# Optimization experiments

Measured on AMD Instinct MI355X. Metric: run time of the kernel, lower is better.

## Reference

```python
import jax, jax.numpy as jnp
import numpy as np

NPOINT, RADIUS, NSAMPLE = 1024, 0.4, 32
BN_EPS = 1e-5


def fps(xyz, npoint):
    # xyz: [B, N, 3]. Deterministic start at index 0 (torch uses randint).
    B, N, _ = xyz.shape

    def step(carry, _):
        distance, farthest = carry  # [B,N], [B]
        centroid = jnp.take_along_axis(xyz, farthest[:, None, None], axis=1)  # [B,1,3]
        dist = jnp.sum((xyz - centroid) ** 2, -1)  # [B,N]
        distance = jnp.minimum(distance, dist)
        new_far = jnp.argmax(distance, axis=-1).astype(jnp.int32)
        return (distance, new_far), farthest

    init = (jnp.full((B, N), 1e10, xyz.dtype), jnp.zeros((B,), jnp.int32))
    _, cents = jax.lax.scan(step, init, None, length=npoint)  # [npoint, B]
    return cents.T  # [B, npoint]


def square_distance(src, dst):
    # src [B,S,3], dst [B,N,3] -> [B,S,N]
    d = -2.0 * jnp.einsum('bsc,bnc->bsn', src, dst)
    d = d + jnp.sum(src ** 2, -1)[:, :, None] + jnp.sum(dst ** 2, -1)[:, None, :]
    return jnp.clip(d, 1e-12, None)


def query_ball_point(radius, nsample, xyz, new_xyz):
    B, N, _ = xyz.shape
    S = new_xyz.shape[1]
    sqr = square_distance(new_xyz, xyz)  # [B,S,N]
    gi = jnp.where(sqr > radius ** 2, N, jnp.arange(N, dtype=jnp.int32)[None, None, :])
    gi = jnp.sort(gi, axis=-1)[:, :, :nsample]  # [B,S,K]
    first = gi[:, :, :1]
    return jnp.where(gi == N, first, gi)


def gather_points(points, idx):
    # points [B,N,C], idx [B,S,K] -> [B,S,K,C]
    B, S, K = idx.shape
    C = points.shape[-1]
    flat = jnp.take_along_axis(points, idx.reshape(B, S * K)[:, :, None], axis=1)
    return flat.reshape(B, S, K, C)


def setup_inputs() -> dict:
    key = jax.random.key(0)
    ks = jax.random.split(key, 10)
    B, N, D = 8, 4096, 64
    inp = {
        'xyz': jax.random.normal(ks[0], (B, 3, N), jnp.float32),
        'points': jax.random.normal(ks[1], (B, D, N), jnp.float32),
    }
    chans = [67, 64, 64, 128]
    for i in range(3):
        cin, cout = chans[i], chans[i + 1]
        inp[f'W{i}'] = jax.random.normal(ks[2 + i], (cout, cin), jnp.float32) * (1.0 / np.sqrt(cin))
        inp[f'b{i}'] = jnp.zeros((cout,), jnp.float32)
        inp[f'g{i}'] = jnp.ones((cout,), jnp.float32)
        inp[f'bt{i}'] = jnp.zeros((cout,), jnp.float32)
    return inp


def _forward(xyz, points, Ws, bs, gs, bts):
    xyz_t = jnp.transpose(xyz, (0, 2, 1))      # [B,N,3]
    pts_t = jnp.transpose(points, (0, 2, 1))   # [B,N,D]
    B, N, _ = xyz_t.shape

    fps_idx = fps(xyz_t, NPOINT)                              # [B,S]
    new_xyz = jnp.take_along_axis(xyz_t, fps_idx[:, :, None], axis=1)  # [B,S,3]
    idx = query_ball_point(RADIUS, NSAMPLE, xyz_t, new_xyz)   # [B,S,K]

    grouped_xyz = gather_points(xyz_t, idx)                   # [B,S,K,3]
    grouped_xyz_norm = grouped_xyz - new_xyz[:, :, None, :]
    grouped_pts = gather_points(pts_t, idx)                   # [B,S,K,D]
    new_points = jnp.concatenate([grouped_xyz_norm, grouped_pts], -1)  # [B,S,K,3+D]

    x = jnp.transpose(new_points, (0, 3, 2, 1))  # [B,C,K,S]
    for W, b, g, bt in zip(Ws, bs, gs, bts):
        x = jnp.einsum('oc,bcks->boks', W, x) + b[None, :, None, None]
        mean = jnp.mean(x, axis=(0, 2, 3), keepdims=True)
        var = jnp.var(x, axis=(0, 2, 3), keepdims=True)
        x = (x - mean) * jax.lax.rsqrt(var + BN_EPS)
        x = x * g[None, :, None, None] + bt[None, :, None, None]
        x = jax.nn.relu(x)
    out = jnp.max(x, axis=2)                      # [B,C_out,S]
    return jnp.transpose(new_xyz, (0, 2, 1)), out


def reference(xyz, points, W0, b0, g0, bt0, W1, b1, g1, bt1, W2, b2, g2, bt2):
    return _forward(xyz, points, (W0, W1, W2), (b0, b1, b2), (g0, g1, g2), (bt0, bt1, bt2))
```

## Files before the change

kernel.cpp:

```cpp
#include <hip/hip_runtime.h>
#include <cstddef>
#include <cstdint>

#define NB 8
#define NPTS 4096
#define NS 1024
#define NK 32
#define ND 64

typedef __attribute__((ext_vector_type(8))) short bf16x8;
typedef __attribute__((ext_vector_type(4))) float f32x4;

__device__ __forceinline__ short f2bf(float f) {
  unsigned u = __float_as_uint(f);
  u += 0x7FFF + ((u >> 16) & 1);
  return (short)(u >> 16);
}

__device__ __forceinline__ float bf2f(unsigned short u) {
  return __uint_as_float((unsigned)u << 16);
}

#define DPP_IMAX(v, ctrl)                                                     \
  {                                                                           \
    int _o = __builtin_amdgcn_update_dpp(v, v, ctrl, 0xf, 0xf, false);        \
    v = (_o > v) ? _o : v;                                                    \
  }

#define DPP_U64MAX(hi, lo, ctrl)                                              \
  {                                                                           \
    unsigned _nh = (unsigned)__builtin_amdgcn_update_dpp((int)(hi), (int)(hi),\
                                                         ctrl, 0xf, 0xf, false);\
    unsigned _nl = (unsigned)__builtin_amdgcn_update_dpp((int)(lo), (int)(lo),\
                                                         ctrl, 0xf, 0xf, false);\
    bool _gt = (_nh > (hi)) || (_nh == (hi) && _nl > (lo));                   \
    hi = _gt ? _nh : (hi);                                                    \
    lo = _gt ? _nl : (lo);                                                    \
  }

#define DPP_RED16(v, OP)                                                      \
  {                                                                           \
    int _i;                                                                   \
    _i = __builtin_amdgcn_update_dpp(__float_as_int(v), __float_as_int(v), 0x111, 0xf, 0xf, false); \
    v = OP(v, __int_as_float(_i));                                            \
    _i = __builtin_amdgcn_update_dpp(__float_as_int(v), __float_as_int(v), 0x112, 0xf, 0xf, false); \
    v = OP(v, __int_as_float(_i));                                            \
    _i = __builtin_amdgcn_update_dpp(__float_as_int(v), __float_as_int(v), 0x114, 0xf, 0xf, false); \
    v = OP(v, __int_as_float(_i));                                            \
    _i = __builtin_amdgcn_update_dpp(__float_as_int(v), __float_as_int(v), 0x118, 0xf, 0xf, false); \
    v = OP(v, __int_as_float(_i));                                            \
  }

__device__ __forceinline__ float fadd_op(float a, float b) { return a + b; }

__global__ __launch_bounds__(512) void fps_pgemm_kernel(
    const float* __restrict__ xyz, float* __restrict__ out_newxyz,
    float* __restrict__ ws_newxyz, const float* __restrict__ points,
    const float* __restrict__ W0, const float* __restrict__ b0g,
    unsigned short* __restrict__ P1) {
  __shared__ __align__(16) char smem[69760];
  const int t = threadIdx.x;

  if (blockIdx.x < 8) {
    float4* sXYZ4 = (float4*)smem;
    volatile unsigned long long* vRed =
        (volatile unsigned long long*)(smem + 65536);
    int* sWidx = (int*)(smem + 65664);
    const int b = blockIdx.x;
    const int wave = t >> 6;
    const int lane = t & 63;
    const float* xb = xyz + (size_t)b * 3 * NPTS;

    for (int i = t; i < NPTS; i += 512) {
      sXYZ4[i] = make_float4(xb[i], xb[NPTS + i], xb[2 * NPTS + i], 0.f);
    }
    if (t == 0) sWidx[0] = 0;
    if (t < 16) vRed[t] = 0xFFFFFFFFFFFFFFFFull;

    float px[8], py[8], pz[8], dist[8];
    {
      float4 a0 = ((const float4*)xb)[2 * t];
      float4 a1 = ((const float4*)xb)[2 * t + 1];
      float4 b0v = ((const float4*)(xb + NPTS))[2 * t];
      float4 b1v = ((const float4*)(xb + NPTS))[2 * t + 1];
      float4 c0 = ((const float4*)(xb + 2 * NPTS))[2 * t];
      float4 c1 = ((const float4*)(xb + 2 * NPTS))[2 * t + 1];
      px[0] = a0.x; px[1] = a0.y; px[2] = a0.z; px[3] = a0.w;
      px[4] = a1.x; px[5] = a1.y; px[6] = a1.z; px[7] = a1.w;
      py[0] = b0v.x; py[1] = b0v.y; py[2] = b0v.z; py[3] = b0v.w;
      py[4] = b1v.x; py[5] = b1v.y; py[6] = b1v.z; py[7] = b1v.w;
      pz[0] = c0.x; pz[1] = c0.y; pz[2] = c0.z; pz[3] = c0.w;
      pz[4] = c1.x; pz[5] = c1.y; pz[6] = c1.z; pz[7] = c1.w;
    }
#pragma unroll
    for (int j = 0; j < 8; ++j) dist[j] = 1e10f;

    float cx = xb[0], cy = xb[NPTS], cz = xb[2 * NPTS];

    __syncthreads();

    for (int s = 0; s < NS - 1; ++s) {
#pragma unroll
      for (int j = 0; j < 8; ++j) {
        float dx = __fadd_rn(px[j], -cx);
        float dy = __fadd_rn(py[j], -cy);
        float dz = __fadd_rn(pz[j], -cz);
        float d = __fadd_rn(__fadd_rn(__fmul_rn(dx, dx), __fmul_rn(dy, dy)),
                            __fmul_rn(dz, dz));
        dist[j] = fminf(dist[j], d);
      }
      float m = fmaxf(fmaxf(fmaxf(dist[0], dist[1]), fmaxf(dist[2], dist[3])),
                      fmaxf(fmaxf(dist[4], dist[5]), fmaxf(dist[6], dist[7])));
      int v = __float_as_int(m);
      DPP_IMAX(v, 0x111)
      DPP_IMAX(v, 0x112)
      DPP_IMAX(v, 0x114)
      DPP_IMAX(v, 0x118)
      DPP_IMAX(v, 0x142)
      DPP_IMAX(v, 0x143)
      const int wm_i = __builtin_amdgcn_readlane(v, 63);
      const float wm = __int_as_float(wm_i);
      unsigned long long claim = __ballot(m == wm);
      int firstlane = __ffsll(claim) - 1;
      const int par = s & 1;
      if (lane == firstlane) {
        int j = 7;
#pragma unroll
        for (int jj = 6; jj >= 0; --jj)
          if (dist[jj] == wm) j = jj;
        unsigned widx = (unsigned)(t * 8 + j);
        unsigned lo = ((unsigned)s << 12) | (4095u - widx);
        vRed[par * 8 + wave] =
            ((unsigned long long)(unsigned)wm_i << 32) | (unsigned long long)lo;
      }
      unsigned long long k;
      for (;;) {
        k = vRed[par * 8 + (lane & 7)];
        bool ok = (((unsigned)k) >> 12) == (unsigned)s;
        if (__ballot(ok) == ~0ull) break;
      }
      unsigned h2 = (unsigned)(k >> 32), l2 = (unsigned)k;
      float4 scoord;
      if (lane < 8) scoord = sXYZ4[4095 - (int)(l2 & 0xFFFu)];
      DPP_U64MAX(h2, l2, 0x111)
      DPP_U64MAX(h2, l2, 0x112)
      DPP_U64MAX(h2, l2, 0x114)
      const unsigned gl = (unsigned)__builtin_amdgcn_readlane((int)l2, 7);
      const int widx = 4095 - (int)(gl & 0xFFFu);
      const int wslot = widx >> 9;
      cx = __int_as_float(__builtin_amdgcn_readlane(__float_as_int(scoord.x), wslot));
      cy = __int_as_float(__builtin_amdgcn_readlane(__float_as_int(scoord.y), wslot));
      cz = __int_as_float(__builtin_amdgcn_readlane(__float_as_int(scoord.z), wslot));
      if (t == 0) sWidx[s + 1] = widx;
    }
    __syncthreads();
    for (int s2 = t; s2 < NS; s2 += 512) {
      int w = sWidx[s2];
      float4 c = sXYZ4[w];
      out_newxyz[b * 3 * NS + s2] = c.x;
      out_newxyz[b * 3 * NS + NS + s2] = c.y;
      out_newxyz[b * 3 * NS + 2 * NS + s2] = c.z;
      ws_newxyz[((b << 10) + s2) * 3 + 0] = c.x;
      ws_newxyz[((b << 10) + s2) * 3 + 1] = c.y;
      ws_newxyz[((b << 10) + s2) * 3 + 2] = c.z;
    }
  } else {
    float* sP = (float*)smem;
    float* sW = (float*)(smem + 16384);
    float* sB = (float*)(smem + 33792);
    const int blk = blockIdx.x - 8;
    const int bb = blk >> 6;
    const int n0 = (blk & 63) * 64;
    const float* pb = points + (size_t)bb * ND * NPTS;
    for (int f = t; f < 4096; f += 512) {
      int c = f >> 6, n = f & 63;
      sP[f] = pb[c * NPTS + n0 + n];
    }
    for (int f = t; f < 4096; f += 512) {
      int c = f >> 6, o = f & 63;
      sW[c * 68 + o] = W0[o * 67 + 3 + c];
    }
    if (t < 64) sB[t] = b0g[t];
    __syncthreads();
    if (t < 256) {
      const int nl = (t & 15) * 4;
      const int ol = (t >> 4) * 4;
      float acc[4][4];
#pragma unroll
      for (int i = 0; i < 4; ++i)
#pragma unroll
        for (int j = 0; j < 4; ++j) acc[i][j] = 0.f;
#pragma unroll 4
      for (int c = 0; c < 64; ++c) {
        float4 xv = *(const float4*)(sP + c * 64 + nl);
        float4 wv = *(const float4*)(sW + c * 68 + ol);
        float xa[4] = {xv.x, xv.y, xv.z, xv.w};
        float wa[4] = {wv.x, wv.y, wv.z, wv.w};
#pragma unroll
        for (int i = 0; i < 4; ++i)
#pragma unroll
          for (int j = 0; j < 4; ++j) acc[i][j] += xa[i] * wa[j];
      }
#pragma unroll
      for (int i = 0; i < 4; ++i) {
        ushort4 v;
        v.x = (unsigned short)f2bf(acc[i][0] + sB[ol + 0]);
        v.y = (unsigned short)f2bf(acc[i][1] + sB[ol + 1]);
        v.z = (unsigned short)f2bf(acc[i][2] + sB[ol + 2]);
        v.w = (unsigned short)f2bf(acc[i][3] + sB[ol + 3]);
        *(ushort4*)(P1 + ((size_t)(bb << 12) + n0 + nl + i) * 64 + ol) = v;
      }
    }
  }
}

__global__ __launch_bounds__(256) void query_gstats_kernel(
    const float* __restrict__ xyz, const float* __restrict__ ws_newxyz,
    const unsigned short* __restrict__ P1, const float* __restrict__ W0,
    unsigned short* __restrict__ y0g, float* __restrict__ partials) {
  const int w = threadIdx.x >> 6;
  const int lane = threadIdx.x & 63;
  const int p = blockIdx.x * 4 + w;
  const int b = p >> 10;
  __shared__ int sIdx[4][32];
  __shared__ float sWS[4][64];
  __shared__ float sWQ[4][64];
  const float* xb = xyz + (size_t)b * 3 * NPTS;
  const float cx = ws_newxyz[p * 3 + 0];
  const float cy = ws_newxyz[p * 3 + 1];
  const float cz = ws_newxyz[p * 3 + 2];
  const float ss = __fadd_rn(__fadd_rn(__fmul_rn(cx, cx), __fmul_rn(cy, cy)), __fmul_rn(cz, cz));
  const float r2 = (float)(0.4 * 0.4);
  int cnt = 0;
  for (int ci = 0; ci < 64 && cnt < 32; ++ci) {
    int n = ci * 64 + lane;
    float x = xb[n], y = xb[NPTS + n], z = xb[2 * NPTS + n];
    float dot = __fadd_rn(__fadd_rn(__fmul_rn(cx, x), __fmul_rn(cy, y)), __fmul_rn(cz, z));
    float dd = __fadd_rn(__fadd_rn(__fmul_rn(x, x), __fmul_rn(y, y)), __fmul_rn(z, z));
    float d = __fmul_rn(-2.0f, dot);
    d = __fadd_rn(d, ss);
    d = __fadd_rn(d, dd);
    d = fmaxf(d, 1e-12f);
    bool inc = (d <= r2);
    unsigned long long m = __ballot(inc);
    int slot = cnt + (int)__popcll(m & ((1ull << lane) - 1ull));
    if (inc && slot < 32) sIdx[w][slot] = n;
    cnt += (int)__popcll(m);
  }
  if (lane < 32) {
    int v;
    if (lane < cnt) v = sIdx[w][lane];
    else v = (cnt > 0) ? sIdx[w][0] : 0;
    sIdx[w][lane] = v;
  }
  const float wx = W0[lane * 67 + 0];
  const float wy = W0[lane * 67 + 1];
  const float wz = W0[lane * 67 + 2];
  float ssum = 0.f, ssq = 0.f;
  unsigned short* y0p = y0g + (size_t)p * 2048;
  for (int r = 0; r < 32; ++r) {
    const int n = sIdx[w][r];
    float P1v = bf2f(P1[((size_t)(b << 12) + n) * 64 + lane]);
    float dx = __fadd_rn(xb[n], -cx);
    float dy = __fadd_rn(xb[NPTS + n], -cy);
    float dz = __fadd_rn(xb[2 * NPTS + n], -cz);
    float y = P1v + (dx * wx + dy * wy + dz * wz);
    y0p[r * 64 + lane] = (unsigned short)f2bf(y);
    ssum += y;
    ssq += y * y;
  }
  sWS[w][lane] = ssum;
  sWQ[w][lane] = ssq;
  __syncthreads();
  const int t = threadIdx.x;
  if (t < 64) {
    float s1 = sWS[0][t] + sWS[1][t] + sWS[2][t] + sWS[3][t];
    float s2 = sWQ[0][t] + sWQ[1][t] + sWQ[2][t] + sWQ[3][t];
    partials[(size_t)blockIdx.x * 128 + t] = s1;
    partials[(size_t)blockIdx.x * 128 + 64 + t] = s2;
  }
}

__global__ __launch_bounds__(256) void conv1_mfma_kernel(
    const unsigned short* __restrict__ y0, const float* __restrict__ W1,
    const float* __restrict__ b1, const float* __restrict__ scaleA,
    const float* __restrict__ shiftA, unsigned short* __restrict__ y1,
    float* __restrict__ partials) {
  __shared__ __align__(16) short sW1b[64 * 72];
  __shared__ __align__(16) short sXb[128 * 72];
  __shared__ float sScale[64], sShift[64], sBias[64];

  const int t = threadIdx.x;
  const int wv = t >> 6, lane = t & 63;
  const int quad = lane >> 4, l15 = lane & 15;
  const int pair0 = blockIdx.x * 4;

  if (t < 64) { sScale[t] = scaleA[t]; sShift[t] = shiftA[t]; sBias[t] = b1[t]; }
  for (int f = t; f < 4096; f += 256) sW1b[(f >> 6) * 72 + (f & 63)] = f2bf(W1[f]);
  __syncthreads();

  const unsigned short* y0b = y0 + (size_t)pair0 * 2048;
  for (int f = t; f < 2048; f += 256) {
    ushort4 v4 = ((const ushort4*)y0b)[f];
    const int row = f >> 4, c4 = (f & 15) * 4;
    short4 o4;
    o4.x = f2bf(fmaxf(bf2f(v4.x) * sScale[c4 + 0] + sShift[c4 + 0], 0.f));
    o4.y = f2bf(fmaxf(bf2f(v4.y) * sScale[c4 + 1] + sShift[c4 + 1], 0.f));
    o4.z = f2bf(fmaxf(bf2f(v4.z) * sScale[c4 + 2] + sShift[c4 + 2], 0.f));
    o4.w = f2bf(fmaxf(bf2f(v4.w) * sScale[c4 + 3] + sShift[c4 + 3], 0.f));
    *(short4*)(sXb + row * 72 + c4) = o4;
  }
  __syncthreads();

  f32x4 acc[8];
#pragma unroll
  for (int i = 0; i < 8; ++i) acc[i] = (f32x4){0.f, 0.f, 0.f, 0.f};
#pragma unroll
  for (int kh = 0; kh < 2; ++kh) {
    const int kc = kh * 32 + quad * 8;
    bf16x8 A = *(const bf16x8*)(sW1b + (wv * 16 + l15) * 72 + kc);
#pragma unroll
    for (int ti = 0; ti < 8; ++ti) {
      bf16x8 B = *(const bf16x8*)(sXb + (ti * 16 + l15) * 72 + kc);
      acc[ti] = __builtin_amdgcn_mfma_f32_16x16x32_bf16(A, B, acc[ti], 0, 0, 0);
    }
  }

#pragma unroll
  for (int reg = 0; reg < 4; ++reg) {
    const int m = wv * 16 + quad * 4 + reg;
    const float bb = sBias[m];
    float v[8];
#pragma unroll
    for (int ti = 0; ti < 8; ++ti) {
      v[ti] = acc[ti][reg] + bb;
      y1[(size_t)(pair0 + (ti >> 1)) * 2048 + m * 32 + (ti & 1) * 16 + l15] =
          (unsigned short)f2bf(v[ti]);
    }
    float s1 = ((v[0] + v[1]) + (v[2] + v[3])) + ((v[4] + v[5]) + (v[6] + v[7]));
    float s2 = ((v[0] * v[0] + v[1] * v[1]) + (v[2] * v[2] + v[3] * v[3])) +
               ((v[4] * v[4] + v[5] * v[5]) + (v[6] * v[6] + v[7] * v[7]));
    DPP_RED16(s1, fadd_op)
    DPP_RED16(s2, fadd_op)
    if (l15 == 15) {
      partials[(size_t)blockIdx.x * 128 + m] = s1;
      partials[(size_t)blockIdx.x * 128 + 64 + m] = s2;
    }
  }
}

__global__ __launch_bounds__(256) void conv2_mfma_kernel(
    const unsigned short* __restrict__ y1, const float* __restrict__ W2,
    const float* __restrict__ b2, const float* __restrict__ scaleA,
    const float* __restrict__ shiftA, float* __restrict__ pmaxT,
    float* __restrict__ pminT, float* __restrict__ partials) {
  __shared__ __align__(16) short sW2[128 * 72];
  __shared__ __align__(16) short sXb[128 * 72];
  __shared__ float sScale[64], sShift[64], sBias[128];

  const int t = threadIdx.x;
  const int pair0 = blockIdx.x * 4;
  const int lane = t & 63;
  const int wv = t >> 6;
  const int quad = lane >> 4;
  const int l15 = lane & 15;

  if (t < 64) { sScale[t] = scaleA[t]; sShift[t] = shiftA[t]; }
  if (t < 128) sBias[t] = b2[t];
  __syncthreads();
  for (int f = t; f < 8192; f += 256) {
    int o = f >> 6, c = f & 63;
    sW2[o * 72 + c] = f2bf(W2[f]);
  }
  for (int f = t; f < 8192; f += 256) {
    int si = f >> 11;
    int rmd = f & 2047;
    int o = rmd >> 5, k = rmd & 31;
    float v = bf2f(y1[(size_t)(pair0 + si) * 2048 + rmd]);
    v = v * sScale[o] + sShift[o];
    v = fmaxf(v, 0.f);
    sXb[(si * 32 + k) * 72 + o] = f2bf(v);
  }
  __syncthreads();

  f32x4 acc[2][8];
#pragma unroll
  for (int i = 0; i < 2; ++i)
#pragma unroll
    for (int ti = 0; ti < 8; ++ti) acc[i][ti] = (f32x4){0.f, 0.f, 0.f, 0.f};
#pragma unroll
  for (int kh = 0; kh < 2; ++kh) {
    const int kc = kh * 32 + quad * 8;
    bf16x8 A0 = *(const bf16x8*)(sW2 + (wv * 32 + l15) * 72 + kc);
    bf16x8 A1 = *(const bf16x8*)(sW2 + (wv * 32 + 16 + l15) * 72 + kc);
#pragma unroll
    for (int ti = 0; ti < 8; ++ti) {
      bf16x8 B = *(const bf16x8*)(sXb + (ti * 16 + l15) * 72 + kc);
      acc[0][ti] = __builtin_amdgcn_mfma_f32_16x16x32_bf16(A0, B, acc[0][ti], 0, 0, 0);
      acc[1][ti] = __builtin_amdgcn_mfma_f32_16x16x32_bf16(A1, B, acc[1][ti], 0, 0, 0);
    }
  }

#pragma unroll
  for (int i = 0; i < 2; ++i) {
#pragma unroll
    for (int reg = 0; reg < 4; ++reg) {
      const int m = wv * 32 + i * 16 + quad * 4 + reg;
      const float bb = sBias[m];
      float v[8];
#pragma unroll
      for (int ti = 0; ti < 8; ++ti) v[ti] = acc[i][ti][reg] + bb;
      float s1 = ((v[0] + v[1]) + (v[2] + v[3])) + ((v[4] + v[5]) + (v[6] + v[7]));
      float s2 = ((v[0] * v[0] + v[1] * v[1]) + (v[2] * v[2] + v[3] * v[3])) +
                 ((v[4] * v[4] + v[5] * v[5]) + (v[6] * v[6] + v[7] * v[7]));
      DPP_RED16(s1, fadd_op)
      DPP_RED16(s2, fadd_op)
      if (l15 == 15) {
        partials[(size_t)blockIdx.x * 256 + m] = s1;
        partials[(size_t)blockIdx.x * 256 + 128 + m] = s2;
      }
#pragma unroll
      for (int si = 0; si < 4; ++si) {
        float mx = fmaxf(v[2 * si], v[2 * si + 1]);
        float mn = fminf(v[2 * si], v[2 * si + 1]);
        DPP_RED16(mx, fmaxf)
        DPP_RED16(mn, fminf)
        if (l15 == 15) {
          pmaxT[(size_t)m * 8192 + pair0 + si] = mx;
          pminT[(size_t)m * 8192 + pair0 + si] = mn;
        }
      }
    }
  }
}

template <int COUT>
__global__ __launch_bounds__(256) void stats_kernel(const float* __restrict__ partials,
                                                    int nblocks,
                                                    const float* __restrict__ gA,
                                                    const float* __restrict__ btA,
                                                    float* __restrict__ scaleA,
                                                    float* __restrict__ shiftA) {
  const int o = blockIdx.x;
  const int t = threadIdx.x;
  double s1 = 0.0, s2 = 0.0;
  for (int blk = t; blk < nblocks; blk += 256) {
    s1 += (double)partials[(size_t)blk * (COUT * 2) + o];
    s2 += (double)partials[(size_t)blk * (COUT * 2) + COUT + o];
  }
  __shared__ double r1[256], r2[256];
  r1[t] = s1; r2[t] = s2;
  __syncthreads();
  for (int st = 128; st > 0; st >>= 1) {
    if (t < st) { r1[t] += r1[t + st]; r2[t] += r2[t + st]; }
    __syncthreads();
  }
  if (t == 0) {
    const double Nr = 262144.0;
    double mean = r1[0] / Nr;
    double var = r2[0] / Nr - mean * mean;
    double rstd = 1.0 / sqrt(var + 1e-5);
    double sc = rstd * (double)gA[o];
    scaleA[o] = (float)sc;
    shiftA[o] = (float)((double)btA[o] - mean * sc);
  }
}

__global__ __launch_bounds__(256) void stats_final_kernel(
    const float* __restrict__ partials, int nblocks,
    const float* __restrict__ pmaxT, const float* __restrict__ pminT,
    const float* __restrict__ gA, const float* __restrict__ btA,
    float* __restrict__ out) {
  const int o = blockIdx.x;
  const int t = threadIdx.x;
  double s1 = 0.0, s2 = 0.0;
  for (int blk = t; blk < nblocks; blk += 256) {
    s1 += (double)partials[(size_t)blk * 256 + o];
    s2 += (double)partials[(size_t)blk * 256 + 128 + o];
  }
  __shared__ double r1[256], r2[256];
  __shared__ float sMean, sRstd;
  r1[t] = s1; r2[t] = s2;
  __syncthreads();
  for (int st = 128; st > 0; st >>= 1) {
    if (t < st) { r1[t] += r1[t + st]; r2[t] += r2[t + st]; }
    __syncthreads();
  }
  if (t == 0) {
    const double Nr = 262144.0;
    double mean = r1[0] / Nr;
    double var = r2[0] / Nr - mean * mean;
    sMean = (float)mean;
    sRstd = (float)(1.0 / sqrt(var + 1e-5));
  }
  __syncthreads();
  const float mn = sMean, rs = sRstd, gg = gA[o], bb = btA[o];
  const float slope = rs * gg;
  const float* src = (slope >= 0.f) ? pmaxT : pminT;
  for (int i = t; i < NB * NS; i += 256) {
    int b = i >> 10;
    int s = i & 1023;
    float v = src[(size_t)o * 8192 + i];
    float t1 = (v - mn) * rs;
    float t2 = t1 * gg + bb;
    out[(size_t)b * (128 * NS) + o * NS + s] = fmaxf(t2, 0.f);
  }
}

extern "C" void kernel_launch(void* const* d_in, const int* in_sizes, int n_in,
                              void* d_out, int out_size, void* d_ws, size_t ws_size,
                              hipStream_t stream) {
  (void)in_sizes; (void)n_in; (void)out_size; (void)ws_size;
  const float* xyz = (const float*)d_in[0];
  const float* points = (const float*)d_in[1];
  const float* W0 = (const float*)d_in[2];
  const float* b0 = (const float*)d_in[3];
  const float* g0 = (const float*)d_in[4];
  const float* bt0 = (const float*)d_in[5];
  const float* W1 = (const float*)d_in[6];
  const float* b1 = (const float*)d_in[7];
  const float* g1 = (const float*)d_in[8];
  const float* bt1 = (const float*)d_in[9];
  const float* W2 = (const float*)d_in[10];
  const float* b2 = (const float*)d_in[11];
  const float* g2 = (const float*)d_in[12];
  const float* bt2 = (const float*)d_in[13];
  float* out = (float*)d_out;

  float* ws = (float*)d_ws;
  size_t off = 0;
  float* newxyz = ws + off;  off += (size_t)NB * NS * 3;
  unsigned short* P1 = (unsigned short*)(ws + off);
  off += (size_t)NB * NPTS * 64;
  unsigned short* y0 = (unsigned short*)(ws + off);
  off += (size_t)8192 * 1024;
  unsigned short* y1 = (unsigned short*)(ws + off);
  off += (size_t)NB * NS * 1024;
  float* partials = ws + off; off += (size_t)8192 * 256;
  float* scaleA = ws + off;  off += 128;
  float* shiftA = ws + off;  off += 128;
  float* pmaxT = ws + off;   off += (size_t)128 * NB * NS;
  float* pminT = ws + off;   off += (size_t)128 * NB * NS;

  fps_pgemm_kernel<<<520, 512, 0, stream>>>(xyz, out, newxyz, points, W0, b0, P1);
  query_gstats_kernel<<<2048, 256, 0, stream>>>(xyz, newxyz, P1, W0, y0, partials);
  stats_kernel<64><<<64, 256, 0, stream>>>(partials, 2048, g0, bt0, scaleA, shiftA);
  conv1_mfma_kernel<<<2048, 256, 0, stream>>>(y0, W1, b1, scaleA, shiftA, y1,
                                              partials);
  stats_kernel<64><<<64, 256, 0, stream>>>(partials, 2048, g1, bt1, scaleA, shiftA);
  conv2_mfma_kernel<<<2048, 256, 0, stream>>>(y1, W2, b2, scaleA, shiftA,
                                              pmaxT, pminT, partials);
  stats_final_kernel<<<128, 256, 0, stream>>>(partials, 2048, pmaxT, pminT,
                                              g2, bt2, out + NB * NS * 3);
}
```

Measured before the change: 884.2 us.

## Fuse ball query into FPS kernel with progress flags to overlap stages

```diff
diff --git a/kernel.cpp b/kernel.cpp
--- a/kernel.cpp
+++ b/kernel.cpp
@@ -53,12 +53,14 @@
 
 __device__ __forceinline__ float fadd_op(float a, float b) { return a + b; }
 
-__global__ __launch_bounds__(512) void fps_pgemm_kernel(
+__global__ __launch_bounds__(512) void fps_pgemm_query_kernel(
     const float* __restrict__ xyz, float* __restrict__ out_newxyz,
     float* __restrict__ ws_newxyz, const float* __restrict__ points,
     const float* __restrict__ W0, const float* __restrict__ b0g,
-    unsigned short* __restrict__ P1) {
-  __shared__ __align__(16) char smem[69760];
+    unsigned short* __restrict__ P1, unsigned short* __restrict__ y0g,
+    float* __restrict__ partials, int* __restrict__ prog,
+    int* __restrict__ pdone) {
+  __shared__ __align__(16) char smem[82048];
   const int t = threadIdx.x;
 
   if (blockIdx.x < 8) {
@@ -152,132 +154,157 @@
       cy = __int_as_float(__builtin_amdgcn_readlane(__float_as_int(scoord.y), wslot));
       cz = __int_as_float(__builtin_amdgcn_readlane(__float_as_int(scoord.z), wslot));
       if (t == 0) sWidx[s + 1] = widx;
+      if ((s & 63) == 63) {
+        if (t < 64) {
+          int w = sWidx[(s - 63) + t];
+          float4 c = sXYZ4[w];
+          float* dst = ws_newxyz + ((size_t)((b << 10) + (s - 63) + t)) * 3;
+          dst[0] = c.x; dst[1] = c.y; dst[2] = c.z;
+        }
+        if (t == 0)
+          __hip_atomic_store(&prog[b], s + 1, __ATOMIC_RELEASE,
+                             __HIP_MEMORY_SCOPE_AGENT);
+      }
     }
     __syncthreads();
+    if (t < 64) {
+      int w = sWidx[960 + t];
+      float4 c = sXYZ4[w];
+      float* dst = ws_newxyz + ((size_t)((b << 10) + 960 + t)) * 3;
+      dst[0] = c.x; dst[1] = c.y; dst[2] = c.z;
+    }
+    if (t == 0)
+      __hip_atomic_store(&prog[b], 1024, __ATOMIC_RELEASE,
+                         __HIP_MEMORY_SCOPE_AGENT);
     for (int s2 = t; s2 < NS; s2 += 512) {
       int w = sWidx[s2];
       float4 c = sXYZ4[w];
       out_newxyz[b * 3 * NS + s2] = c.x;
       out_newxyz[b * 3 * NS + NS + s2] = c.y;
       out_newxyz[b * 3 * NS + 2 * NS + s2] = c.z;
-      ws_newxyz[((b << 10) + s2) * 3 + 0] = c.x;
-      ws_newxyz[((b << 10) + s2) * 3 + 1] = c.y;
-      ws_newxyz[((b << 10) + s2) * 3 + 2] = c.z;
     }
   } else {
+    const int i = blockIdx.x - 8;
     float* sP = (float*)smem;
     float* sW = (float*)(smem + 16384);
     float* sB = (float*)(smem + 33792);
-    const int blk = blockIdx.x - 8;
-    const int bb = blk >> 6;
-    const int n0 = (blk & 63) * 64;
-    const float* pb = points + (size_t)bb * ND * NPTS;
-    for (int f = t; f < 4096; f += 512) {
-      int c = f >> 6, n = f & 63;
-      sP[f] = pb[c * NPTS + n0 + n];
-    }
-    for (int f = t; f < 4096; f += 512) {
-      int c = f >> 6, o = f & 63;
-      sW[c * 68 + o] = W0[o * 67 + 3 + c];
-    }
     if (t < 64) sB[t] = b0g[t];
+    int ntiles = 0;
+    for (int tile = i; tile < 512; tile += 248) {
+      ++ntiles;
+      const int bb = tile >> 6;
+      const int n0 = (tile & 63) * 64;
+      const float* pb = points + (size_t)bb * ND * NPTS;
+      __syncthreads();
+      for (int f = t; f < 4096; f += 512) {
+        int c = f >> 6, n = f & 63;
+        sP[f] = pb[c * NPTS + n0 + n];
+      }
+      for (int f = t; f < 4096; f += 512) {
+        int c = f >> 6, o = f & 63;
+        sW[c * 68 + o] = W0[o * 67 + 3 + c];
+      }
+      __syncthreads();
+      if (t < 256) {
+        const int nl = (t & 15) * 4;
+        const int ol = (t >> 4) * 4;
+        float acc[4][4];
+#pragma unroll
+        for (int a = 0; a < 4; ++a)
+#pragma unroll
+          for (int j = 0; j < 4; ++j) acc[a][j] = 0.f;
+#pragma unroll 4
+        for (int c = 0; c < 64; ++c) {
+          float4 xv = *(const float4*)(sP + c * 64 + nl);
+          float4 wv = *(const float4*)(sW + c * 68 + ol);
+          float xa[4] = {xv.x, xv.y, xv.z, xv.w};
+          float wa[4] = {wv.x, wv.y, wv.z, wv.w};
+#pragma unroll
+          for (int a = 0; a < 4; ++a)
+#pragma unroll
+            for (int j = 0; j < 4; ++j) acc[a][j] += xa[a] * wa[j];
+        }
+#pragma unroll
+        for (int a = 0; a < 4; ++a) {
+          ushort4 v;
+          v.x = (unsigned short)f2bf(acc[a][0] + sB[ol + 0]);
+          v.y = (unsigned short)f2bf(acc[a][1] + sB[ol + 1]);
+          v.z = (unsigned short)f2bf(acc[a][2] + sB[ol + 2]);
+          v.w = (unsigned short)f2bf(acc[a][3] + sB[ol + 3]);
+          *(ushort4*)(P1 + ((size_t)(bb << 12) + n0 + nl + a) * 64 + ol) = v;
+        }
+      }
+    }
     __syncthreads();
-    if (t < 256) {
-      const int nl = (t & 15) * 4;
-      const int ol = (t >> 4) * 4;
-      float acc[4][4];
-#pragma unroll
-      for (int i = 0; i < 4; ++i)
-#pragma unroll
-        for (int j = 0; j < 4; ++j) acc[i][j] = 0.f;
-#pragma unroll 4
-      for (int c = 0; c < 64; ++c) {
-        float4 xv = *(const float4*)(sP + c * 64 + nl);
-        float4 wv = *(const float4*)(sW + c * 68 + ol);
-        float xa[4] = {xv.x, xv.y, xv.z, xv.w};
-        float wa[4] = {wv.x, wv.y, wv.z, wv.w};
-#pragma unroll
-        for (int i = 0; i < 4; ++i)
-#pragma unroll
-          for (int j = 0; j < 4; ++j) acc[i][j] += xa[i] * wa[j];
-      }
-#pragma unroll
-      for (int i = 0; i < 4; ++i) {
-        ushort4 v;
-        v.x = (unsigned short)f2bf(acc[i][0] + sB[ol + 0]);
-        v.y = (unsigned short)f2bf(acc[i][1] + sB[ol + 1]);
-        v.z = (unsigned short)f2bf(acc[i][2] + sB[ol + 2]);
-        v.w = (unsigned short)f2bf(acc[i][3] + sB[ol + 3]);
-        *(ushort4*)(P1 + ((size_t)(bb << 12) + n0 + nl + i) * 64 + ol) = v;
-      }
-    }
-  }
-}
-
-__global__ __launch_bounds__(256) void query_gstats_kernel(
-    const float* __restrict__ xyz, const float* __restrict__ ws_newxyz,
-    const unsigned short* __restrict__ P1, const float* __restrict__ W0,
-    unsigned short* __restrict__ y0g, float* __restrict__ partials) {
-  const int w = threadIdx.x >> 6;
-  const int lane = threadIdx.x & 63;
-  const int p = blockIdx.x * 4 + w;
-  const int b = p >> 10;
-  __shared__ int sIdx[4][32];
-  __shared__ float sWS[4][64];
-  __shared__ float sWQ[4][64];
-  const float* xb = xyz + (size_t)b * 3 * NPTS;
-  const float cx = ws_newxyz[p * 3 + 0];
-  const float cy = ws_newxyz[p * 3 + 1];
-  const float cz = ws_newxyz[p * 3 + 2];
-  const float ss = __fadd_rn(__fadd_rn(__fmul_rn(cx, cx), __fmul_rn(cy, cy)), __fmul_rn(cz, cz));
-  const float r2 = (float)(0.4 * 0.4);
-  int cnt = 0;
-  for (int ci = 0; ci < 64 && cnt < 32; ++ci) {
-    int n = ci * 64 + lane;
-    float x = xb[n], y = xb[NPTS + n], z = xb[2 * NPTS + n];
-    float dot = __fadd_rn(__fadd_rn(__fmul_rn(cx, x), __fmul_rn(cy, y)), __fmul_rn(cz, z));
-    float dd = __fadd_rn(__fadd_rn(__fmul_rn(x, x), __fmul_rn(y, y)), __fmul_rn(z, z));
-    float d = __fmul_rn(-2.0f, dot);
-    d = __fadd_rn(d, ss);
-    d = __fadd_rn(d, dd);
-    d = fmaxf(d, 1e-12f);
-    bool inc = (d <= r2);
-    unsigned long long m = __ballot(inc);
-    int slot = cnt + (int)__popcll(m & ((1ull << lane) - 1ull));
-    if (inc && slot < 32) sIdx[w][slot] = n;
-    cnt += (int)__popcll(m);
-  }
-  if (lane < 32) {
-    int v;
-    if (lane < cnt) v = sIdx[w][lane];
-    else v = (cnt > 0) ? sIdx[w][0] : 0;
-    sIdx[w][lane] = v;
-  }
-  const float wx = W0[lane * 67 + 0];
-  const float wy = W0[lane * 67 + 1];
-  const float wz = W0[lane * 67 + 2];
-  float ssum = 0.f, ssq = 0.f;
-  unsigned short* y0p = y0g + (size_t)p * 2048;
-  for (int r = 0; r < 32; ++r) {
-    const int n = sIdx[w][r];
-    float P1v = bf2f(P1[((size_t)(b << 12) + n) * 64 + lane]);
-    float dx = __fadd_rn(xb[n], -cx);
-    float dy = __fadd_rn(xb[NPTS + n], -cy);
-    float dz = __fadd_rn(xb[2 * NPTS + n], -cz);
-    float y = P1v + (dx * wx + dy * wy + dz * wz);
-    y0p[r * 64 + lane] = (unsigned short)f2bf(y);
-    ssum += y;
-    ssq += y * y;
-  }
-  sWS[w][lane] = ssum;
-  sWQ[w][lane] = ssq;
-  __syncthreads();
-  const int t = threadIdx.x;
-  if (t < 64) {
-    float s1 = sWS[0][t] + sWS[1][t] + sWS[2][t] + sWS[3][t];
-    float s2 = sWQ[0][t] + sWQ[1][t] + sWQ[2][t] + sWQ[3][t];
-    partials[(size_t)blockIdx.x * 128 + t] = s1;
-    partials[(size_t)blockIdx.x * 128 + 64 + t] = s2;
+    if (t == 0)
+      __hip_atomic_fetch_add(pdone, ntiles, __ATOMIC_RELEASE,
+                             __HIP_MEMORY_SCOPE_AGENT);
+    while (__hip_atomic_load(pdone, __ATOMIC_ACQUIRE,
+                             __HIP_MEMORY_SCOPE_AGENT) < 512) {
+      __builtin_amdgcn_s_sleep(2);
+    }
+    __syncthreads();
+
+    const int wavei = t >> 6;
+    const int lane = t & 63;
+    int* sIdxW = (int*)smem + wavei * 32;
+    const float wx = W0[lane * 67 + 0];
+    const float wy = W0[lane * 67 + 1];
+    const float wz = W0[lane * 67 + 2];
+    const float r2 = (float)(0.4 * 0.4);
+    for (int p = i * 8 + wavei; p < 8192; p += 1984) {
+      const int b = p >> 10;
+      const int s = p & 1023;
+      while (__hip_atomic_load(&prog[b], __ATOMIC_ACQUIRE,
+                               __HIP_MEMORY_SCOPE_AGENT) <= s) {
+        __builtin_amdgcn_s_sleep(32);
+      }
+      const float* xb = xyz + (size_t)b * 3 * NPTS;
+      const float cx = ws_newxyz[p * 3 + 0];
+      const float cy = ws_newxyz[p * 3 + 1];
+      const float cz = ws_newxyz[p * 3 + 2];
+      const float ss = __fadd_rn(
+          __fadd_rn(__fmul_rn(cx, cx), __fmul_rn(cy, cy)), __fmul_rn(cz, cz));
+      int cnt = 0;
+      for (int ci = 0; ci < 64 && cnt < 32; ++ci) {
+        int n = ci * 64 + lane;
+        float x = xb[n], y = xb[NPTS + n], z = xb[2 * NPTS + n];
+        float dot = __fadd_rn(__fadd_rn(__fmul_rn(cx, x), __fmul_rn(cy, y)),
+                              __fmul_rn(cz, z));
+        float dd = __fadd_rn(__fadd_rn(__fmul_rn(x, x), __fmul_rn(y, y)),
+                             __fmul_rn(z, z));
+        float d = __fmul_rn(-2.0f, dot);
+        d = __fadd_rn(d, ss);
+        d = __fadd_rn(d, dd);
+        d = fmaxf(d, 1e-12f);
+        bool inc = (d <= r2);
+        unsigned long long m = __ballot(inc);
+        int slot = cnt + (int)__popcll(m & ((1ull << lane) - 1ull));
+        if (inc && slot < 32) sIdxW[slot] = n;
+        cnt += (int)__popcll(m);
+      }
+      if (lane < 32) {
+        int v;
+        if (lane < cnt) v = sIdxW[lane];
+        else v = (cnt > 0) ? sIdxW[0] : 0;
+        sIdxW[lane] = v;
+      }
+      float ssum = 0.f, ssq = 0.f;
+      unsigned short* y0p = y0g + (size_t)p * 2048;
+      for (int r = 0; r < 32; ++r) {
+        const int n = sIdxW[r];
+        float P1v = bf2f(P1[((size_t)(b << 12) + n) * 64 + lane]);
+        float dx = __fadd_rn(xb[n], -cx);
+        float dy = __fadd_rn(xb[NPTS + n], -cy);
+        float dz = __fadd_rn(xb[2 * NPTS + n], -cz);
+        float y = P1v + (dx * wx + dy * wy + dz * wz);
+        y0p[r * 64 + lane] = (unsigned short)f2bf(y);
+        ssum += y;
+        ssq += y * y;
+      }
+      partials[(size_t)p * 128 + lane] = ssum;
+      partials[(size_t)p * 128 + 64 + lane] = ssq;
+    }
   }
 }
 
@@ -541,10 +568,20 @@
   float* shiftA = ws + off;  off += 128;
   float* pmaxT = ws + off;   off += (size_t)128 * NB * NS;
   float* pminT = ws + off;   off += (size_t)128 * NB * NS;
-
-  fps_pgemm_kernel<<<520, 512, 0, stream>>>(xyz, out, newxyz, points, W0, b0, P1);
-  query_gstats_kernel<<<2048, 256, 0, stream>>>(xyz, newxyz, P1, W0, y0, partials);
-  stats_kernel<64><<<64, 256, 0, stream>>>(partials, 2048, g0, bt0, scaleA, shiftA);
+  int* prog = (int*)(ws + off); off += 16;
+  int* pdone = prog + 8;
+
+  hipMemsetAsync(prog, 0, 64, stream);
+
+  {
+    void* kargs[] = {(void*)&xyz,  (void*)&out,      (void*)&newxyz,
+                     (void*)&points, (void*)&W0,     (void*)&b0,
+                     (void*)&P1,   (void*)&y0,       (void*)&partials,
+                     (void*)&prog, (void*)&pdone};
+    hipLaunchCooperativeKernel(fps_pgemm_query_kernel, dim3(256), dim3(512),
+                               kargs, 0, stream);
+  }
+  stats_kernel<64><<<64, 256, 0, stream>>>(partials, 8192, g0, bt0, scaleA, shiftA);
   conv1_mfma_kernel<<<2048, 256, 0, stream>>>(y0, W1, b1, scaleA, shiftA, y1,
                                               partials);
   stats_kernel<64><<<64, 256, 0, stream>>>(partials, 2048, g1, bt1, scaleA, shiftA);
```

Measured after the change: 1.063 ms. 20.2% more time.
